# Performance work log

Measured on AMD Instinct MI355X. Metric: run time of the kernel, lower is better.

## Reference

```python
import jax, jax.numpy as jnp
import numpy as np
import math

B, L, I, H = 32, 2048, 64, 512
HALF = H // 2
DT = 0.05
RHO = 0.99
INPUT_SCALING = 1.0
STD = 1.0
GAMMA_MIN, GAMMA_MAX = 0.5, 1.0
EPS_MIN, EPS_MAX = 0.5, 1.0


def setup_inputs() -> dict:
    key = jax.random.key(0)
    ks = jax.random.split(key, 7)
    x = jax.random.normal(ks[0], (B, L, I), dtype=jnp.float32)
    x2h = jax.random.uniform(ks[1], (I, H), dtype=jnp.float32) * INPUT_SCALING
    h2h = 2.0 * (2.0 * jax.random.uniform(ks[2], (H, H), dtype=jnp.float32) - 1.0)
    # spectral_norm_scaling: rescale so largest singular value == rho
    h2h = h2h * (RHO / jnp.linalg.norm(h2h, ord=2))
    bias = (2.0 * jax.random.uniform(ks[3], (H,), dtype=jnp.float32) - 1.0) * INPUT_SCALING
    gamma = jax.random.uniform(ks[4], (H,), dtype=jnp.float32) * (GAMMA_MAX - GAMMA_MIN) + GAMMA_MIN
    epsilon = jax.random.uniform(ks[5], (H,), dtype=jnp.float32) * (EPS_MAX - EPS_MIN) + EPS_MIN
    # RandomFourierFeature: W_sin = W_cos, shape [half_dim, in_dim]
    W_rff = jax.random.normal(ks[6], (HALF, H), dtype=jnp.float32) * STD
    return {"x": x, "x2h": x2h, "h2h": h2h, "bias": bias,
            "gamma": gamma, "epsilon": epsilon, "W_rff": W_rff}


def _run(x, x2h, h2h, bias, gamma, epsilon, W_rff):
    b = x.shape[0]
    inv_sqrt_half = 1.0 / math.sqrt(HALF)

    def step(carry, xt):
        hy, hz, zsum = carry
        pre = jnp.tanh(xt @ x2h + hy @ h2h + bias)          # [B,H]
        hz = hz + DT * (pre - gamma * hy - epsilon * hz)
        hy = hy + DT * hz
        wx = hy @ W_rff.T                                   # [B,HALF]
        z = jnp.concatenate([jnp.cos(wx), jnp.sin(wx)], axis=-1) * inv_sqrt_half
        return (hy, hz, zsum + z), None

    hy0 = jnp.zeros((b, H), dtype=x.dtype)
    hz0 = jnp.zeros((b, H), dtype=x.dtype)
    zsum0 = jnp.zeros((b, H), dtype=x.dtype)
    (hy, hz, zsum), _ = jax.lax.scan(step, (hy0, hz0, zsum0), jnp.swapaxes(x, 0, 1))
    mu = zsum / x.shape[1]  # mean over time of per-step RFF states
    return mu, hy


def reference(x, x2h, h2h, bias, gamma, epsilon, W_rff):
    return _run(x, x2h, h2h, bias, gamma, epsilon, W_rff)
```

## Files before the change

### kernel.cpp

```cpp
#include <hip/hip_runtime.h>
#include <math.h>

#define Bz 32
#define Lz 2048
#define Iz 64
#define Hz 512
#define HALFz 256
#define DTz 0.05f
#define NMEM 8
#define NBLK 256
#define TPB 512

typedef unsigned long long u64;

__device__ __forceinline__ bool tagok(u64 v, unsigned tag) {
  u64 want = (u64)tag | ((u64)tag << 48);
  return ((v ^ want) & 0xFFFF00000000FFFFull) == 0ull;
}
__device__ __forceinline__ u64 packv(float f, unsigned tag) {
  return (u64)tag | ((u64)__float_as_uint(f) << 16) | ((u64)tag << 48);
}
__device__ __forceinline__ float unpackv(u64 v) {
  return __uint_as_float((unsigned)(v >> 16));
}

__device__ __forceinline__ u64 load_sc0(const u64* p) {
  u64 r;
  asm volatile("global_load_dwordx2 %0, %1, off sc0\n\t"
               "s_waitcnt vmcnt(0)"
               : "=&v"(r) : "v"(p) : "memory");
  return r;
}
__device__ __forceinline__ void store_sc0(u64* p, u64 v) {
  asm volatile("global_store_dwordx2 %0, %1, off sc0"
               :: "v"(p), "v"(v) : "memory");
}

__global__ __launch_bounds__(TPB, 1) void coesn_xg(
    const float* __restrict__ x, const float* __restrict__ x2h,
    const float* __restrict__ h2h, const float* __restrict__ bias,
    const float* __restrict__ gam, const float* __restrict__ eps,
    const float* __restrict__ W_rff, unsigned* __restrict__ regs,
    u64* __restrict__ Xb, u64* __restrict__ Yb, float* __restrict__ out) {
  extern __shared__ float lds_force[];
  __shared__ __align__(16) float hyf[2][Hz];
  __shared__ __align__(16) float xbuf[2][Iz];
  __shared__ int sbm[2];

  const int u = threadIdx.x;

  if (u == 0) {
    unsigned xcc = __builtin_amdgcn_s_getreg((31 << 11) | 20) & 7u;
    unsigned idx = __hip_atomic_fetch_add(regs + xcc, 1u, __ATOMIC_RELAXED,
                                          __HIP_MEMORY_SCOPE_AGENT);
    __hip_atomic_fetch_add(regs + 32, 1u, __ATOMIC_RELEASE,
                           __HIP_MEMORY_SCOPE_AGENT);
    unsigned v;
    do { v = __hip_atomic_load(regs + 32, __ATOMIC_ACQUIRE,
                               __HIP_MEMORY_SCOPE_AGENT); } while (v < NBLK);
    unsigned n[8], full[8], rem[8], totf = 0;
    for (int i = 0; i < 8; ++i) {
      n[i] = __hip_atomic_load(regs + i, __ATOMIC_RELAXED,
                               __HIP_MEMORY_SCOPE_AGENT);
      full[i] = n[i] >> 3; rem[i] = n[i] & 7; totf += full[i];
    }
    int gid, mem;
    if (idx < 8u * full[xcc]) {
      unsigned pf = 0;
      for (unsigned i = 0; i < xcc; ++i) pf += full[i];
      gid = (int)(pf + (idx >> 3)); mem = (int)(idx & 7u);
    } else {
      unsigned pr = 0;
      for (unsigned i = 0; i < xcc; ++i) pr += rem[i];
      unsigned rank = pr + (idx - 8u * full[xcc]);
      gid = (int)(totf + (rank >> 3)); mem = (int)(rank & 7u);
    }
    sbm[0] = gid; sbm[1] = mem;
  }
  __syncthreads();
  const int b = sbm[0];
  const int m = sbm[1];

  const int w  = u >> 6;
  const int l  = u & 63;
  const int c0 = m * 64;
  const int j  = ((l & 1) << 2) | (l & 2) | ((l >> 2) & 1);
  const int mycol = c0 + w * 8 + j;
  const int rloc = u >> 4, kseg = u & 15;

  float wreg[8][8];
  {
    const float* hrow = h2h + (size_t)(8 * l) * Hz + c0 + 8 * w;
    #pragma unroll
    for (int r = 0; r < 8; ++r) {
      float4 v0 = *(const float4*)(hrow + (size_t)r * Hz);
      float4 v1 = *(const float4*)(hrow + (size_t)r * Hz + 4);
      wreg[r][0] = v0.x; wreg[r][1] = v0.y; wreg[r][2] = v0.z; wreg[r][3] = v0.w;
      wreg[r][4] = v1.x; wreg[r][5] = v1.y; wreg[r][6] = v1.z; wreg[r][7] = v1.w;
    }
  }
  float xreg[8];
  {
    float4 v0 = *(const float4*)(x2h + (size_t)l * Hz + c0 + 8 * w);
    float4 v1 = *(const float4*)(x2h + (size_t)l * Hz + c0 + 8 * w + 4);
    xreg[0] = v0.x; xreg[1] = v0.y; xreg[2] = v0.z; xreg[3] = v0.w;
    xreg[4] = v1.x; xreg[5] = v1.y; xreg[6] = v1.z; xreg[7] = v1.w;
  }
  float wr[32];
  {
    const float* wp = W_rff + (size_t)(m * 32 + rloc) * Hz + kseg * 32;
    #pragma unroll
    for (int i = 0; i < 32; ++i) wr[i] = wp[i];
  }

  const float bu = bias[mycol];
  const float gu = gam[mycol];
  const float eu = eps[mycol];
  float hy = 0.f, hz = 0.f, zc = 0.f, zs = 0.f;
  hyf[0][u] = 0.f;
  if (u < 16) ((float4*)xbuf[0])[u] = ((const float4*)(x + (size_t)b * Lz * Iz))[u];
  __syncthreads();

  auto rff_acc = [&](const float* hsrc) {
    float acc = 0.f;
    const float4* hp = (const float4*)hsrc;
    #pragma unroll
    for (int i = 0; i < 8; ++i) {
      int q = kseg * 8 + i;
      float4 h4 = hp[q ^ ((q >> 3) & 7)];
      acc = fmaf(h4.x, wr[4 * i], acc);
      acc = fmaf(h4.y, wr[4 * i + 1], acc);
      acc = fmaf(h4.z, wr[4 * i + 2], acc);
      acc = fmaf(h4.w, wr[4 * i + 3], acc);
    }
    acc += __shfl_xor(acc, 1); acc += __shfl_xor(acc, 2);
    acc += __shfl_xor(acc, 4); acc += __shfl_xor(acc, 8);
    float sv, cv;
    __sincosf(acc, &sv, &cv);
    zc += cv; zs += sv;
  };

  for (int t = 0; t < Lz; ++t) {
    const int cur = t & 1, nxt = cur ^ 1;

    if (u < 16 && t + 1 < Lz)
      ((float4*)xbuf[nxt])[u] =
          ((const float4*)(x + ((size_t)b * Lz + (t + 1)) * Iz))[u];

    float hv[8];
    {
      const float4* hp = (const float4*)hyf[cur];
      int q0 = 2 * l, q1 = 2 * l + 1;
      float4 h0 = hp[q0 ^ ((q0 >> 3) & 7)];
      float4 h1 = hp[q1 ^ ((q1 >> 3) & 7)];
      hv[0] = h0.x; hv[1] = h0.y; hv[2] = h0.z; hv[3] = h0.w;
      hv[4] = h1.x; hv[5] = h1.y; hv[6] = h1.z; hv[7] = h1.w;
    }
    float a[8] = {0.f,0.f,0.f,0.f,0.f,0.f,0.f,0.f};
    #pragma unroll
    for (int r = 0; r < 8; ++r) {
      float h = hv[r];
      #pragma unroll
      for (int c = 0; c < 8; ++c) a[c] = fmaf(h, wreg[r][c], a[c]);
    }
    {
      float xv = xbuf[cur][l];
      #pragma unroll
      for (int c = 0; c < 8; ++c) a[c] = fmaf(xv, xreg[c], a[c]);
    }
    #pragma unroll
    for (int i = 0; i < 4; ++i) {
      float snd = (l & 1) ? a[i] : a[i + 4];
      float rcv = __shfl_xor(snd, 1);
      a[i] = ((l & 1) ? a[i + 4] : a[i]) + rcv;
    }
    #pragma unroll
    for (int i = 0; i < 2; ++i) {
      float snd = (l & 2) ? a[i] : a[i + 2];
      float rcv = __shfl_xor(snd, 2);
      a[i] = ((l & 2) ? a[i + 2] : a[i]) + rcv;
    }
    float s;
    {
      float snd = (l & 4) ? a[0] : a[1];
      float rcv = __shfl_xor(snd, 4);
      s = ((l & 4) ? a[1] : a[0]) + rcv;
    }
    s += __shfl_xor(s, 8); s += __shfl_xor(s, 16); s += __shfl_xor(s, 32);

    s += bu;
    float e2 = __expf(s + s);
    float pre = 1.f - 2.f * __builtin_amdgcn_rcpf(e2 + 1.f);
    float hzn = fmaf(DTz, pre - gu * hy - eu * hz, hz);
    hy = fmaf(DTz, hzn, hy);
    hz = hzn;

    const unsigned tag = (unsigned)(t + 1);
    u64* XA = Xb + ((size_t)nxt * Bz + b) * Hz;
    u64* YA = Yb + ((size_t)nxt * Bz + b) * Hz;

    u64 pv = packv(hy, tag);
    if (l < 8) store_sc0(XA + mycol, pv);

    u64 spec = 0;
    if (w != m)
      asm volatile("global_load_dwordx2 %0, %1, off sc0"
                   : "=&v"(spec) : "v"(XA + u) : "memory");

    if (l < 8) {
      __hip_atomic_store(YA + mycol, pv, __ATOMIC_RELAXED,
                         __HIP_MEMORY_SCOPE_AGENT);
      int q = mycol >> 2;
      hyf[nxt][((q ^ ((q >> 3) & 7)) << 2) | (mycol & 3)] = hy;
    }

    if (t > 0) rff_acc(hyf[cur]);

    if (w != m) {
      asm volatile("s_waitcnt vmcnt(1)" : "+v"(spec) :: "memory");
      u64 v = spec;
      if (!tagok(v, tag)) {
        long it = 0;
        for (;;) {
          v = load_sc0(XA + u);
          if (tagok(v, tag)) break;
          if (it & 1) {
            v = __hip_atomic_load(YA + u, __ATOMIC_RELAXED,
                                  __HIP_MEMORY_SCOPE_AGENT);
            if (tagok(v, tag)) break;
          }
          if (++it > (1 << 20)) break;
        }
      }
      int q = u >> 2;
      hyf[nxt][((q ^ ((q >> 3) & 7)) << 2) | (u & 3)] = unpackv(v);
    }
    __syncthreads();
  }

  rff_acc(hyf[0]);

  if (l < 8) out[(size_t)Bz * Hz + (size_t)b * Hz + mycol] = hy;
  if (kseg == 0) {
    const float sc = 0.0625f / 2048.f;
    out[(size_t)b * Hz + m * 32 + rloc] = zc * sc;
    out[(size_t)b * Hz + HALFz + m * 32 + rloc] = zs * sc;
  }
}

__global__ __launch_bounds__(TPB, 2) void coesn_x2(
    const float* __restrict__ x, const float* __restrict__ x2h,
    const float* __restrict__ h2h, const float* __restrict__ bias,
    const float* __restrict__ gam, const float* __restrict__ eps,
    const float* __restrict__ W_rff, u64* __restrict__ Xb,
    u64* __restrict__ Yb, float* __restrict__ out) {
  __shared__ __align__(16) float hyf[2][Hz];
  __shared__ __align__(16) float xb[2][Iz];

  const int b  = blockIdx.x & 31;
  const int m  = blockIdx.x >> 5;
  const int u  = threadIdx.x;
  const int w  = u >> 6;
  const int l  = u & 63;
  const int c0 = m * 64;
  const int j  = ((l & 1) << 2) | (l & 2) | ((l >> 2) & 1);
  const int mycol = c0 + w * 8 + j;
  const int rloc = u >> 4, kseg = u & 15;

  float wreg[8][8];
  {
    const float* hrow = h2h + (size_t)(8 * l) * Hz + c0 + 8 * w;
    #pragma unroll
    for (int r = 0; r < 8; ++r) {
      float4 v0 = *(const float4*)(hrow + (size_t)r * Hz);
      float4 v1 = *(const float4*)(hrow + (size_t)r * Hz + 4);
      wreg[r][0] = v0.x; wreg[r][1] = v0.y; wreg[r][2] = v0.z; wreg[r][3] = v0.w;
      wreg[r][4] = v1.x; wreg[r][5] = v1.y; wreg[r][6] = v1.z; wreg[r][7] = v1.w;
    }
  }
  float xreg[8];
  {
    float4 v0 = *(const float4*)(x2h + (size_t)l * Hz + c0 + 8 * w);
    float4 v1 = *(const float4*)(x2h + (size_t)l * Hz + c0 + 8 * w + 4);
    xreg[0] = v0.x; xreg[1] = v0.y; xreg[2] = v0.z; xreg[3] = v0.w;
    xreg[4] = v1.x; xreg[5] = v1.y; xreg[6] = v1.z; xreg[7] = v1.w;
  }
  float wr[32];
  {
    const float* wp = W_rff + (size_t)(m * 32 + rloc) * Hz + kseg * 32;
    #pragma unroll
    for (int i = 0; i < 32; ++i) wr[i] = wp[i];
  }

  const float bu = bias[mycol];
  const float gu = gam[mycol];
  const float eu = eps[mycol];
  float hy = 0.f, hz = 0.f, zc = 0.f, zs = 0.f;
  hyf[0][u] = 0.f;
  if (u < 16) ((float4*)xb[0])[u] = ((const float4*)(x + (size_t)b * Lz * Iz))[u];
  __syncthreads();

  auto rff_acc = [&](const float* hsrc) {
    float acc = 0.f;
    const float4* hp = (const float4*)hsrc;
    #pragma unroll
    for (int i = 0; i < 8; ++i) {
      int q = kseg * 8 + i;
      float4 h4 = hp[q ^ ((q >> 3) & 7)];
      acc = fmaf(h4.x, wr[4 * i], acc);
      acc = fmaf(h4.y, wr[4 * i + 1], acc);
      acc = fmaf(h4.z, wr[4 * i + 2], acc);
      acc = fmaf(h4.w, wr[4 * i + 3], acc);
    }
    acc += __shfl_xor(acc, 1); acc += __shfl_xor(acc, 2);
    acc += __shfl_xor(acc, 4); acc += __shfl_xor(acc, 8);
    float sv, cv;
    __sincosf(acc, &sv, &cv);
    zc += cv; zs += sv;
  };

  for (int t = 0; t < Lz; ++t) {
    const int cur = t & 1, nxt = cur ^ 1;
    if (u < 16 && t + 1 < Lz)
      ((float4*)xb[nxt])[u] =
          ((const float4*)(x + ((size_t)b * Lz + (t + 1)) * Iz))[u];
    float hv[8];
    {
      const float4* hp = (const float4*)hyf[cur];
      int q0 = 2 * l, q1 = 2 * l + 1;
      float4 h0 = hp[q0 ^ ((q0 >> 3) & 7)];
      float4 h1 = hp[q1 ^ ((q1 >> 3) & 7)];
      hv[0] = h0.x; hv[1] = h0.y; hv[2] = h0.z; hv[3] = h0.w;
      hv[4] = h1.x; hv[5] = h1.y; hv[6] = h1.z; hv[7] = h1.w;
    }
    float a[8] = {0.f,0.f,0.f,0.f,0.f,0.f,0.f,0.f};
    #pragma unroll
    for (int r = 0; r < 8; ++r) {
      float h = hv[r];
      #pragma unroll
      for (int c = 0; c < 8; ++c) a[c] = fmaf(h, wreg[r][c], a[c]);
    }
    {
      float xv = xb[cur][l];
      #pragma unroll
      for (int c = 0; c < 8; ++c) a[c] = fmaf(xv, xreg[c], a[c]);
    }
    #pragma unroll
    for (int i = 0; i < 4; ++i) {
      float snd = (l & 1) ? a[i] : a[i + 4];
      float rcv = __shfl_xor(snd, 1);
      a[i] = ((l & 1) ? a[i + 4] : a[i]) + rcv;
    }
    #pragma unroll
    for (int i = 0; i < 2; ++i) {
      float snd = (l & 2) ? a[i] : a[i + 2];
      float rcv = __shfl_xor(snd, 2);
      a[i] = ((l & 2) ? a[i + 2] : a[i]) + rcv;
    }
    float s;
    {
      float snd = (l & 4) ? a[0] : a[1];
      float rcv = __shfl_xor(snd, 4);
      s = ((l & 4) ? a[1] : a[0]) + rcv;
    }
    s += __shfl_xor(s, 8); s += __shfl_xor(s, 16); s += __shfl_xor(s, 32);

    s += bu;
    float e2 = __expf(s + s);
    float pre = 1.f - 2.f * __builtin_amdgcn_rcpf(e2 + 1.f);
    float hzn = fmaf(DTz, pre - gu * hy - eu * hz, hz);
    hy = fmaf(DTz, hzn, hy);
    hz = hzn;

    const unsigned tag = (unsigned)(t + 1);
    u64* XA = Xb + ((size_t)nxt * Bz + b) * Hz;
    u64* YA = Yb + ((size_t)nxt * Bz + b) * Hz;

    if (l < 8) {
      u64 pv = packv(hy, tag);
      *(volatile u64*)(XA + mycol) = pv;
      __hip_atomic_store(YA + mycol, pv, __ATOMIC_RELAXED,
                         __HIP_MEMORY_SCOPE_AGENT);
      int q = mycol >> 2;
      hyf[nxt][((q ^ ((q >> 3) & 7)) << 2) | (mycol & 3)] = hy;
    }
    if (t > 0) rff_acc(hyf[cur]);
    if (w != m) {
      u64 v; int it = 0;
      for (;;) {
        v = *(volatile const u64*)(XA + u);
        if (tagok(v, tag)) break;
        if (it >= 2) {
          v = __hip_atomic_load(YA + u, __ATOMIC_RELAXED,
                                __HIP_MEMORY_SCOPE_AGENT);
          if (tagok(v, tag)) break;
        }
        if (++it > (1 << 20)) break;
      }
      int q = u >> 2;
      hyf[nxt][((q ^ ((q >> 3) & 7)) << 2) | (u & 3)] = unpackv(v);
    }
    __syncthreads();
  }

  rff_acc(hyf[0]);
  if (l < 8) out[(size_t)Bz * Hz + (size_t)b * Hz + mycol] = hy;
  if (kseg == 0) {
    const float sc = 0.0625f / 2048.f;
    out[(size_t)b * Hz + m * 32 + rloc] = zc * sc;
    out[(size_t)b * Hz + HALFz + m * 32 + rloc] = zs * sc;
  }
}

#define FMA4(P, S, W) do { (P).x = fmaf((S), (W).x, (P).x); (P).y = fmaf((S), (W).y, (P).y); \
                           (P).z = fmaf((S), (W).z, (P).z); (P).w = fmaf((S), (W).w, (P).w); } while(0)

__global__ __launch_bounds__(512) void coesn_scan_fb(
    const float* __restrict__ x, const float* __restrict__ x2h,
    const float* __restrict__ h2h, const float* __restrict__ bias,
    const float* __restrict__ gam, const float* __restrict__ eps,
    const float* __restrict__ W_rff, float* __restrict__ out) {
  const int b = blockIdx.x;
  const int u = threadIdx.x;
  __shared__ __align__(16) float hy_lds[Hz];
  __shared__ __align__(16) float x_lds[Iz];
  __shared__ float4 part[4][128];
  __shared__ float wx_lds[HALFz];

  float hy = 0.f, hz = 0.f, zsum = 0.f;
  const float bu = bias[u];
  const float gu = gam[u];
  const float eu = eps[u];

  const int kq = u >> 7;
  const int g  = u & 127;
  const int jj = u >> 2;
  const int ks = u & 3;

  const float4* __restrict__ H4 = (const float4*)h2h;
  const float4* __restrict__ X2 = (const float4*)x2h;
  const float4* __restrict__ W4 = (const float4*)W_rff;
  const float4* __restrict__ XG = (const float4*)x;
  const float4* hy4 = (const float4*)hy_lds;

  hy_lds[u] = 0.f;
  if (u < 16) ((float4*)x_lds)[u] = XG[(long)b * Lz * 16 + u];
  __syncthreads();

  for (int t = 0; t < Lz; ++t) {
    float4 p = make_float4(0.f, 0.f, 0.f, 0.f);
    {
      const float4* hp = (const float4*)&hy_lds[kq << 7];
      #pragma unroll 8
      for (int k4 = 0; k4 < 32; ++k4) {
        float4 hv = hp[k4];
        const float4* wr2 = &H4[(size_t)((kq << 7) + (k4 << 2)) * 128 + g];
        float4 w0 = wr2[0]; float4 w1 = wr2[128]; float4 w2 = wr2[256]; float4 w3 = wr2[384];
        FMA4(p, hv.x, w0); FMA4(p, hv.y, w1); FMA4(p, hv.z, w2); FMA4(p, hv.w, w3);
      }
      const float4* xp = (const float4*)&x_lds[kq << 4];
      #pragma unroll
      for (int k4 = 0; k4 < 4; ++k4) {
        float4 xv = xp[k4];
        const float4* wr2 = &X2[(size_t)((kq << 4) + (k4 << 2)) * 128 + g];
        float4 w0 = wr2[0]; float4 w1 = wr2[128]; float4 w2 = wr2[256]; float4 w3 = wr2[384];
        FMA4(p, xv.x, w0); FMA4(p, xv.y, w1); FMA4(p, xv.z, w2); FMA4(p, xv.w, w3);
      }
    }
    part[kq][g] = p;
    __syncthreads();
    {
      const float* pp = (const float*)part;
      float s = (pp[u] + pp[512 + u]) + (pp[1024 + u] + pp[1536 + u]);
      float pre = tanhf(s + bu);
      float hzn = fmaf(DTz, pre - gu * hy - eu * hz, hz);
      hy = fmaf(DTz, hzn, hy);
      hz = hzn;
      hy_lds[u] = hy;
      if (u < 16 && t + 1 < Lz)
        ((float4*)x_lds)[u] = XG[((long)b * Lz + (t + 1)) * 16 + u];
    }
    __syncthreads();
    {
      float4 acc0 = make_float4(0.f,0.f,0.f,0.f), acc1 = make_float4(0.f,0.f,0.f,0.f);
      #pragma unroll 4
      for (int it = 0; it < 32; ++it) {
        int k4 = (it << 2) + ks;
        float4 hv = hy4[k4];
        float4 w0 = W4[(size_t)jj * 128 + k4];
        float4 w1 = W4[(size_t)(jj + 128) * 128 + k4];
        acc0.x = fmaf(hv.x, w0.x, acc0.x); acc0.y = fmaf(hv.y, w0.y, acc0.y);
        acc0.z = fmaf(hv.z, w0.z, acc0.z); acc0.w = fmaf(hv.w, w0.w, acc0.w);
        acc1.x = fmaf(hv.x, w1.x, acc1.x); acc1.y = fmaf(hv.y, w1.y, acc1.y);
        acc1.z = fmaf(hv.z, w1.z, acc1.z); acc1.w = fmaf(hv.w, w1.w, acc1.w);
      }
      float a0 = (acc0.x + acc0.y) + (acc0.z + acc0.w);
      float a1 = (acc1.x + acc1.y) + (acc1.z + acc1.w);
      a0 += __shfl_xor(a0, 1); a0 += __shfl_xor(a0, 2);
      a1 += __shfl_xor(a1, 1); a1 += __shfl_xor(a1, 2);
      if (ks == 0) { wx_lds[jj] = a0; wx_lds[jj + 128] = a1; }
    }
    __syncthreads();
    {
      float v = wx_lds[u & 255];
      zsum += (u < HALFz) ? cosf(v) : sinf(v);
    }
  }
  out[(long)b * Hz + u] = zsum * (0.0625f / 2048.f);
  out[(long)Bz * Hz + (long)b * Hz + u] = hy;
}

extern "C" void kernel_launch(void* const* d_in, const int* in_sizes, int n_in,
                              void* d_out, int out_size, void* d_ws, size_t ws_size,
                              hipStream_t stream) {
  const float* x    = (const float*)d_in[0];
  const float* x2h  = (const float*)d_in[1];
  const float* h2h  = (const float*)d_in[2];
  const float* bias = (const float*)d_in[3];
  const float* gam  = (const float*)d_in[4];
  const float* eps  = (const float*)d_in[5];
  const float* wrff = (const float*)d_in[6];
  float* out = (float*)d_out;

  const size_t NEX = (size_t)2 * Bz * Hz;
  const size_t WS_NEED = 4096 + 2 * NEX * sizeof(u64);
  const unsigned DYN_LDS = 96 * 1024;

  if (ws_size >= WS_NEED) {
    unsigned* regs = (unsigned*)d_ws;
    u64* Xb = (u64*)((char*)d_ws + 4096);
    u64* Yb = Xb + NEX;
    hipMemsetAsync(d_ws, 0, WS_NEED, stream);

    hipError_t ea = hipFuncSetAttribute((const void*)coesn_xg,
                                        hipFuncAttributeMaxDynamicSharedMemorySize,
                                        (int)DYN_LDS);
    if (ea == hipSuccess) {
      void* args[] = { (void*)&x, (void*)&x2h, (void*)&h2h, (void*)&bias,
                       (void*)&gam, (void*)&eps, (void*)&wrff,
                       (void*)&regs, (void*)&Xb, (void*)&Yb, (void*)&out };
      hipError_t e = hipLaunchCooperativeKernel((const void*)coesn_xg,
                                                dim3(NBLK), dim3(TPB),
                                                args, DYN_LDS, stream);
      if (e == hipSuccess) return;
    }

    void* args2[] = { (void*)&x, (void*)&x2h, (void*)&h2h, (void*)&bias,
                      (void*)&gam, (void*)&eps, (void*)&wrff,
                      (void*)&Xb, (void*)&Yb, (void*)&out };
    hipError_t e2 = hipLaunchCooperativeKernel((const void*)coesn_x2,
                                               dim3(Bz * NMEM), dim3(TPB),
                                               args2, 0, stream);
    if (e2 == hipSuccess) return;
  }
  coesn_scan_fb<<<Bz, 512, 0, stream>>>(x, x2h, h2h, bias, gam, eps, wrff, out);
}
```

Baseline: 3.621 ms.

## Replace XCC-aware block placement with single exchange buffer and pipelined polling

Drops the runtime XCC-aware group assignment (atomic registration and a grid-wide spin-wait) and maps blocks to batch and slice directly from blockIdx, with launch bounds relaxed to two blocks per CU and no forced 96KB LDS. The dual X/Y exchange buffers become one buffer, written with an agent-scope atomic store and read with sc0 sc1 loads. Polling now keeps two loads in flight, alternating between them, and the block barrier is a raw s_barrier after an lgkmcnt wait. s_setprio raises priority during the recurrent matvec. The risk is that blocks of one batch may land on different XCDs, making cross-block exchange latency higher than with the old co-location.

After: 4.440 ms. 1.23x slower.

```diff
diff --git a/kernel.cpp b/kernel.cpp
--- a/kernel.cpp
+++ b/kernel.cpp
@@ -8,7 +8,6 @@
 #define HALFz 256
 #define DTz 0.05f
 #define NMEM 8
-#define NBLK 256
 #define TPB 512
 
 typedef unsigned long long u64;
@@ -24,63 +23,18 @@
   return __uint_as_float((unsigned)(v >> 16));
 }
 
-__device__ __forceinline__ u64 load_sc0(const u64* p) {
-  u64 r;
-  asm volatile("global_load_dwordx2 %0, %1, off sc0\n\t"
-               "s_waitcnt vmcnt(0)"
-               : "=&v"(r) : "v"(p) : "memory");
-  return r;
-}
-__device__ __forceinline__ void store_sc0(u64* p, u64 v) {
-  asm volatile("global_store_dwordx2 %0, %1, off sc0"
-               :: "v"(p), "v"(v) : "memory");
-}
-
-__global__ __launch_bounds__(TPB, 1) void coesn_xg(
+__global__ __launch_bounds__(TPB, 2) void coesn_y1(
     const float* __restrict__ x, const float* __restrict__ x2h,
     const float* __restrict__ h2h, const float* __restrict__ bias,
     const float* __restrict__ gam, const float* __restrict__ eps,
-    const float* __restrict__ W_rff, unsigned* __restrict__ regs,
-    u64* __restrict__ Xb, u64* __restrict__ Yb, float* __restrict__ out) {
-  extern __shared__ float lds_force[];
+    const float* __restrict__ W_rff, u64* __restrict__ Eb,
+    float* __restrict__ out) {
   __shared__ __align__(16) float hyf[2][Hz];
-  __shared__ __align__(16) float xbuf[2][Iz];
-  __shared__ int sbm[2];
-
-  const int u = threadIdx.x;
-
-  if (u == 0) {
-    unsigned xcc = __builtin_amdgcn_s_getreg((31 << 11) | 20) & 7u;
-    unsigned idx = __hip_atomic_fetch_add(regs + xcc, 1u, __ATOMIC_RELAXED,
-                                          __HIP_MEMORY_SCOPE_AGENT);
-    __hip_atomic_fetch_add(regs + 32, 1u, __ATOMIC_RELEASE,
-                           __HIP_MEMORY_SCOPE_AGENT);
-    unsigned v;
-    do { v = __hip_atomic_load(regs + 32, __ATOMIC_ACQUIRE,
-                               __HIP_MEMORY_SCOPE_AGENT); } while (v < NBLK);
-    unsigned n[8], full[8], rem[8], totf = 0;
-    for (int i = 0; i < 8; ++i) {
-      n[i] = __hip_atomic_load(regs + i, __ATOMIC_RELAXED,
-                               __HIP_MEMORY_SCOPE_AGENT);
-      full[i] = n[i] >> 3; rem[i] = n[i] & 7; totf += full[i];
-    }
-    int gid, mem;
-    if (idx < 8u * full[xcc]) {
-      unsigned pf = 0;
-      for (unsigned i = 0; i < xcc; ++i) pf += full[i];
-      gid = (int)(pf + (idx >> 3)); mem = (int)(idx & 7u);
-    } else {
-      unsigned pr = 0;
-      for (unsigned i = 0; i < xcc; ++i) pr += rem[i];
-      unsigned rank = pr + (idx - 8u * full[xcc]);
-      gid = (int)(totf + (rank >> 3)); mem = (int)(rank & 7u);
-    }
-    sbm[0] = gid; sbm[1] = mem;
-  }
-  __syncthreads();
-  const int b = sbm[0];
-  const int m = sbm[1];
-
+  __shared__ __align__(16) float xb[2][Iz];
+
+  const int b  = blockIdx.x & 31;
+  const int m  = blockIdx.x >> 5;
+  const int u  = threadIdx.x;
   const int w  = u >> 6;
   const int l  = u & 63;
   const int c0 = m * 64;
@@ -117,8 +71,9 @@
   const float gu = gam[mycol];
   const float eu = eps[mycol];
   float hy = 0.f, hz = 0.f, zc = 0.f, zs = 0.f;
+  u64 v0 = 0, v1 = 0;
   hyf[0][u] = 0.f;
-  if (u < 16) ((float4*)xbuf[0])[u] = ((const float4*)(x + (size_t)b * Lz * Iz))[u];
+  if (u < 16) ((float4*)xb[0])[u] = ((const float4*)(x + (size_t)b * Lz * Iz))[u];
   __syncthreads();
 
   auto rff_acc = [&](const float* hsrc) {
@@ -144,9 +99,10 @@
     const int cur = t & 1, nxt = cur ^ 1;
 
     if (u < 16 && t + 1 < Lz)
-      ((float4*)xbuf[nxt])[u] =
+      ((float4*)xb[nxt])[u] =
           ((const float4*)(x + ((size_t)b * Lz + (t + 1)) * Iz))[u];
 
+    __builtin_amdgcn_s_setprio(1);
     float hv[8];
     {
       const float4* hp = (const float4*)hyf[cur];
@@ -164,7 +120,7 @@
       for (int c = 0; c < 8; ++c) a[c] = fmaf(h, wreg[r][c], a[c]);
     }
     {
-      float xv = xbuf[cur][l];
+      float xv = xb[cur][l];
       #pragma unroll
       for (int c = 0; c < 8; ++c) a[c] = fmaf(xv, xreg[c], a[c]);
     }
@@ -194,21 +150,20 @@
     float hzn = fmaf(DTz, pre - gu * hy - eu * hz, hz);
     hy = fmaf(DTz, hzn, hy);
     hz = hzn;
+    __builtin_amdgcn_s_setprio(0);
 
     const unsigned tag = (unsigned)(t + 1);
-    u64* XA = Xb + ((size_t)nxt * Bz + b) * Hz;
-    u64* YA = Yb + ((size_t)nxt * Bz + b) * Hz;
-
-    u64 pv = packv(hy, tag);
-    if (l < 8) store_sc0(XA + mycol, pv);
-
-    u64 spec = 0;
+    u64* EA = Eb + ((size_t)nxt * Bz + b) * Hz;
+
+    asm volatile("s_waitcnt vmcnt(0)" ::: "memory");
+
     if (w != m)
-      asm volatile("global_load_dwordx2 %0, %1, off sc0"
-                   : "=&v"(spec) : "v"(XA + u) : "memory");
+      asm volatile("global_load_dwordx2 %0, %1, off sc0 sc1"
+                   : "=&v"(v0) : "v"(EA + u) : "memory");
 
     if (l < 8) {
-      __hip_atomic_store(YA + mycol, pv, __ATOMIC_RELAXED,
+      u64 pv = packv(hy, tag);
+      __hip_atomic_store(EA + mycol, pv, __ATOMIC_RELAXED,
                          __HIP_MEMORY_SCOPE_AGENT);
       int q = mycol >> 2;
       hyf[nxt][((q ^ ((q >> 3) & 7)) << 2) | (mycol & 3)] = hy;
@@ -217,26 +172,38 @@
     if (t > 0) rff_acc(hyf[cur]);
 
     if (w != m) {
-      asm volatile("s_waitcnt vmcnt(1)" : "+v"(spec) :: "memory");
-      u64 v = spec;
-      if (!tagok(v, tag)) {
-        long it = 0;
-        for (;;) {
-          v = load_sc0(XA + u);
-          if (tagok(v, tag)) break;
-          if (it & 1) {
-            v = __hip_atomic_load(YA + u, __ATOMIC_RELAXED,
-                                  __HIP_MEMORY_SCOPE_AGENT);
-            if (tagok(v, tag)) break;
-          }
-          if (++it > (1 << 20)) break;
+      asm volatile("global_load_dwordx2 %0, %1, off sc0 sc1"
+                   : "=&v"(v1) : "v"(EA + u) : "memory");
+      u64 val; long it = 0; int sel = 0;
+      for (;;) {
+        u64 got;
+        if (sel == 0) {
+          asm volatile("s_waitcnt vmcnt(1)" : "+v"(v0) :: "memory");
+          got = v0;
+          if (!tagok(got, tag))
+            asm volatile("global_load_dwordx2 %0, %1, off sc0 sc1"
+                         : "=&v"(v0) : "v"(EA + u) : "memory");
+        } else {
+          asm volatile("s_waitcnt vmcnt(1)" : "+v"(v1) :: "memory");
+          got = v1;
+          if (!tagok(got, tag))
+            asm volatile("global_load_dwordx2 %0, %1, off sc0 sc1"
+                         : "=&v"(v1) : "v"(EA + u) : "memory");
         }
+        if (tagok(got, tag)) { val = got; break; }
+        sel ^= 1;
+        if (++it > (1 << 21)) { val = got; break; }
       }
       int q = u >> 2;
-      hyf[nxt][((q ^ ((q >> 3) & 7)) << 2) | (u & 3)] = unpackv(v);
-    }
-    __syncthreads();
-  }
+      hyf[nxt][((q ^ ((q >> 3) & 7)) << 2) | (u & 3)] = unpackv(val);
+    }
+
+    asm volatile("s_waitcnt lgkmcnt(0)" ::: "memory");
+    __builtin_amdgcn_s_barrier();
+  }
+
+  asm volatile("s_waitcnt vmcnt(0)" ::: "memory");
+  asm volatile("" :: "v"(v0), "v"(v1));
 
   rff_acc(hyf[0]);
 
@@ -523,31 +490,23 @@
   float* out = (float*)d_out;
 
   const size_t NEX = (size_t)2 * Bz * Hz;
-  const size_t WS_NEED = 4096 + 2 * NEX * sizeof(u64);
-  const unsigned DYN_LDS = 96 * 1024;
-
+  const size_t WS_NEED = 2 * NEX * sizeof(u64);
   if (ws_size >= WS_NEED) {
-    unsigned* regs = (unsigned*)d_ws;
-    u64* Xb = (u64*)((char*)d_ws + 4096);
-    u64* Yb = Xb + NEX;
+    u64* Eb = (u64*)d_ws;
+    u64* Yb = Eb + NEX;
     hipMemsetAsync(d_ws, 0, WS_NEED, stream);
 
-    hipError_t ea = hipFuncSetAttribute((const void*)coesn_xg,
-                                        hipFuncAttributeMaxDynamicSharedMemorySize,
-                                        (int)DYN_LDS);
-    if (ea == hipSuccess) {
-      void* args[] = { (void*)&x, (void*)&x2h, (void*)&h2h, (void*)&bias,
-                       (void*)&gam, (void*)&eps, (void*)&wrff,
-                       (void*)&regs, (void*)&Xb, (void*)&Yb, (void*)&out };
-      hipError_t e = hipLaunchCooperativeKernel((const void*)coesn_xg,
-                                                dim3(NBLK), dim3(TPB),
-                                                args, DYN_LDS, stream);
-      if (e == hipSuccess) return;
-    }
+    void* args[] = { (void*)&x, (void*)&x2h, (void*)&h2h, (void*)&bias,
+                     (void*)&gam, (void*)&eps, (void*)&wrff,
+                     (void*)&Eb, (void*)&out };
+    hipError_t e = hipLaunchCooperativeKernel((const void*)coesn_y1,
+                                              dim3(Bz * NMEM), dim3(TPB),
+                                              args, 0, stream);
+    if (e == hipSuccess) return;
 
     void* args2[] = { (void*)&x, (void*)&x2h, (void*)&h2h, (void*)&bias,
                       (void*)&gam, (void*)&eps, (void*)&wrff,
-                      (void*)&Xb, (void*)&Yb, (void*)&out };
+                      (void*)&Eb, (void*)&Yb, (void*)&out };
     hipError_t e2 = hipLaunchCooperativeKernel((const void*)coesn_x2,
                                                dim3(Bz * NMEM), dim3(TPB),
                                                args2, 0, stream);
```
